# Performance work log

Hardware: AMD Instinct MI355X
Metric: run time of the kernel (lower is better)

Reference implementation:

```python
import jax, jax.numpy as jnp
import numpy as np

N_HEADS = 4
D_K = 32
C = 128
SCALE = D_K ** (-0.5)


def setup_inputs() -> dict:
    key = jax.random.key(0)
    k1, k2, k3, k4, k5 = jax.random.split(key, 5)
    x = jax.random.normal(k1, (16, C, 32, 32), dtype=jnp.float32)
    # nn.Linear(C, n_heads*d_k*3): weight [out, in], bias [out]
    Wp = jax.random.normal(k2, (N_HEADS * D_K * 3, C), dtype=jnp.float32) * (C ** -0.5)
    bp = jax.random.normal(k3, (N_HEADS * D_K * 3,), dtype=jnp.float32) * 0.01
    # nn.Linear(n_heads*d_k, C)
    Wo = jax.random.normal(k4, (C, N_HEADS * D_K), dtype=jnp.float32) * ((N_HEADS * D_K) ** -0.5)
    bo = jax.random.normal(k5, (C,), dtype=jnp.float32) * 0.01
    return {"x": x, "Wp": Wp, "bp": bp, "Wo": Wo, "bo": bo}


def reference(x, Wp, bp, Wo, bo):
    b, c, h, w = x.shape
    n = h * w
    # (b,c,h,w) -> (b, n, c); NOTE: GroupNorm from __init__ is never applied in forward.
    xf = x.reshape(b, c, n).transpose(0, 2, 1)
    qkv = (xf @ Wp.T + bp).reshape(b, n, N_HEADS, 3 * D_K)
    q, k, v = jnp.split(qkv, 3, axis=-1)  # each (b, n, heads, d_k)
    attn = jnp.einsum('bihd,bjhd->bijh', q, k) * SCALE  # (b, n, n, heads)
    # Faithful to original: softmax over LAST axis = heads axis (original code bug)
    attn = jax.nn.softmax(attn, axis=-1)
    res = jnp.einsum('bijh,bjhd->bihd', attn, v).reshape(b, n, N_HEADS * D_K)
    res = res @ Wo.T + bo + xf
    return res.transpose(0, 2, 1).reshape(b, c, h, w)
```

## Files before the change

### kernel.cpp

```cpp
#include <hip/hip_runtime.h>

typedef short s8v __attribute__((ext_vector_type(8)));
typedef float f4v __attribute__((ext_vector_type(4)));

#define NTOK 1024
#define CD 128
#define QSCALE 0.25506953149031838f

__device__ __forceinline__ ushort f2bf(float x) {
    union { float f; unsigned u; } v; v.f = x;
    unsigned u = v.u + 0x7fff + ((v.u >> 16) & 1);
    return (ushort)(u >> 16);
}
__device__ __forceinline__ float bf2f(ushort x) {
    union { unsigned u; float f; } v; v.u = ((unsigned)x) << 16;
    return v.f;
}
__device__ __forceinline__ void gl_lds16(const ushort* g, ushort* l) {
    __builtin_amdgcn_global_load_lds(
        (const __attribute__((address_space(1))) unsigned int*)(g),
        (__attribute__((address_space(3))) unsigned int*)(l), 16, 0, 0);
}
__device__ __forceinline__ unsigned cvt_pk_bf16(float lo, float hi) {
    unsigned r;
    asm("v_cvt_pk_bf16_f32 %0, %1, %2" : "=v"(r) : "v"(lo), "v"(hi));
    return r;
}

__global__ __launch_bounds__(256) void k_pre(const float* __restrict__ x,
                                             const float* __restrict__ Wp,
                                             const float* __restrict__ Wo,
                                             ushort* __restrict__ xt,
                                             ushort* __restrict__ wpre) {
    const int t = threadIdx.x;
    const int bx = blockIdx.x;
    if (bx < 256) {
        __shared__ ushort tile[128 * 68];
        const int b = bx >> 4;
        const int n0 = (bx & 15) << 6;
        #pragma unroll
        for (int p = 0; p < 8; ++p) {
            const int c = p * 16 + (t >> 4);
            const int n4 = t & 15;
            const float4 v = *(const float4*)&x[(b * CD + c) * NTOK + n0 + n4 * 4];
            ushort4 o;
            o.x = f2bf(v.x); o.y = f2bf(v.y); o.z = f2bf(v.z); o.w = f2bf(v.w);
            *(ushort4*)&tile[c * 68 + n4 * 4] = o;
        }
        __syncthreads();
        #pragma unroll
        for (int p = 0; p < 4; ++p) {
            const int nl = t >> 2;
            const int g = (t & 3) + p * 4;
            s8v tmp;
            #pragma unroll
            for (int e = 0; e < 8; ++e) tmp[e] = (short)tile[(g * 8 + e) * 68 + nl];
            const int n = n0 + nl;
            *(s8v*)&xt[(b * NTOK + n) * CD + ((g ^ (nl & 7)) * 8)] = tmp;
        }
    } else {
        const int kind = bx - 256;
        ushort* dst = wpre + kind * (CD * CD);
        for (int e = t * 4; e < CD * CD; e += 1024) {
            const int f = e >> 7, c = e & 127;
            const float* src;
            if (kind == 3) src = &Wo[f * CD + c];
            else           src = &Wp[((f >> 5) * 96 + kind * 32 + (f & 31)) * CD + c];
            const float4 v = *(const float4*)src;
            ushort4 o;
            o.x = f2bf(v.x); o.y = f2bf(v.y); o.z = f2bf(v.z); o.w = f2bf(v.w);
            *(ushort4*)&dst[f * CD + (((c >> 3) ^ (f & 7)) * 8) + (c & 7)] = o;
        }
    }
}

__global__ __launch_bounds__(256) void k_proj(const ushort* __restrict__ xt,
                                              const ushort* __restrict__ wpre,
                                              const float* __restrict__ bp,
                                              ushort* __restrict__ qb,
                                              ushort* __restrict__ kb,
                                              ushort* __restrict__ vtb) {
    __shared__ ushort Abuf[128 * 128];
    __shared__ ushort Bbuf[64 * 128];
    const int t = threadIdx.x;
    const int lane = t & 63;
    const int w = t >> 6;
    const int li = lane & 15;
    const int lg = lane >> 4;
    const int bx = blockIdx.x;
    const int kind = bx >> 8;
    const int idx = bx & 255;

    const ushort* Asrc;
    const ushort* Bsrc;
    if (kind < 2) {
        Asrc = xt + (idx >> 1) * 128 * CD;
        Bsrc = wpre + kind * (CD * CD) + (idx & 1) * 64 * CD;
    } else {
        Asrc = wpre + 2 * (CD * CD);
        Bsrc = xt + idx * 64 * CD;
    }
    {
        const ushort* ga = Asrc + w * 4096;
        ushort* la = Abuf + w * 4096;
        #pragma unroll
        for (int i = 0; i < 8; ++i) gl_lds16(ga + i * 512 + lane * 8, la + i * 512);
        const ushort* gb = Bsrc + w * 2048;
        ushort* lb = Bbuf + w * 2048;
        #pragma unroll
        for (int i = 0; i < 4; ++i) gl_lds16(gb + i * 512 + lane * 8, lb + i * 512);
    }
    __syncthreads();

    const f4v fz = {0.f, 0.f, 0.f, 0.f};
    f4v acc[2][4];
    #pragma unroll
    for (int mf = 0; mf < 2; ++mf)
        #pragma unroll
        for (int nf = 0; nf < 4; ++nf) acc[mf][nf] = fz;
    const int m_base = w * 32;
    #pragma unroll
    for (int kk = 0; kk < 4; ++kk) {
        s8v a[2], bb[4];
        #pragma unroll
        for (int mf = 0; mf < 2; ++mf) {
            const int row = m_base + mf * 16 + li;
            a[mf] = *(const s8v*)&Abuf[row * CD + (((kk * 4 + lg) ^ (row & 7)) * 8)];
        }
        #pragma unroll
        for (int nf = 0; nf < 4; ++nf) {
            const int row = nf * 16 + li;
            bb[nf] = *(const s8v*)&Bbuf[row * CD + (((kk * 4 + lg) ^ (row & 7)) * 8)];
        }
        #pragma unroll
        for (int mf = 0; mf < 2; ++mf)
            #pragma unroll
            for (int nf = 0; nf < 4; ++nf)
                acc[mf][nf] = __builtin_amdgcn_mfma_f32_16x16x32_bf16(a[mf], bb[nf], acc[mf][nf], 0, 0, 0);
    }

    if (kind < 2) {
        ushort* dst = (kind == 0) ? qb : kb;
        const int m0 = (idx >> 1) * 128;
        const int f0 = (idx & 1) * 64;
        #pragma unroll
        for (int mf = 0; mf < 2; ++mf)
            #pragma unroll
            for (int nf = 0; nf < 4; ++nf) {
                const int f = f0 + nf * 16 + li;
                const int o = (f >> 5) * 96 + kind * 32 + (f & 31);
                const float bias = bp[o];
                #pragma unroll
                for (int r = 0; r < 4; ++r) {
                    const int row = m0 + m_base + mf * 16 + lg * 4 + r;
                    float v = acc[mf][nf][r] + bias;
                    if (kind == 0) v *= QSCALE;
                    dst[row * CD + f] = f2bf(v);
                }
            }
    } else {
        const int n0g = idx * 64;
        const int b = n0g >> 10;
        const int nl0 = n0g & 1023;
        #pragma unroll
        for (int mf = 0; mf < 2; ++mf)
            #pragma unroll
            for (int r = 0; r < 4; ++r) {
                const int f = m_base + mf * 16 + lg * 4 + r;
                const int o = (f >> 5) * 96 + 64 + (f & 31);
                const float bias = bp[o];
                #pragma unroll
                for (int nf = 0; nf < 4; ++nf) {
                    const int n = nl0 + nf * 16 + li;
                    const int jl = n & 31;
                    const int np = (n & ~31) | (((jl & 15) >> 2) * 8 + (jl & 3) + ((jl >> 4) << 2));
                    vtb[(b * CD + f) * NTOK + np] = f2bf(acc[mf][nf][r] + bias);
                }
            }
    }
}

__global__ __launch_bounds__(256) void k_attn(const ushort* __restrict__ qb,
                                              const ushort* __restrict__ kb,
                                              const ushort* __restrict__ vtb,
                                              ushort* __restrict__ res4) {
    __shared__ ushort kbuf[2][32 * 128];
    __shared__ ushort vbuf[2][128 * 40];
    const int t = threadIdx.x;
    const int lane = t & 63;
    const int w = t >> 6;
    const int b = blockIdx.x;
    const int it = blockIdx.y;
    const int js = blockIdx.z;
    const int i0 = it * 64 + w * 16;
    const int li = lane & 15;
    const int lg = lane >> 4;

    s8v qf[4];
    #pragma unroll
    for (int h = 0; h < 4; ++h)
        qf[h] = *(const s8v*)&qb[(b*NTOK + i0 + li)*CD + h*32 + lg*8];

    const f4v fz = {0.f, 0.f, 0.f, 0.f};
    f4v acc[4][2];
    #pragma unroll
    for (int h = 0; h < 4; ++h) { acc[h][0] = fz; acc[h][1] = fz; }

    const int j0 = js * 256;
    const int kr0 = (w*2)*4 + (lane>>4);
    const int kr1 = (w*2+1)*4 + (lane>>4);
    const ushort* ksrc0 = &kb[(b*NTOK + j0 + kr0)*CD + (((lane&15) ^ (kr0&7))*8)];
    const ushort* ksrc1 = &kb[(b*NTOK + j0 + kr1)*CD + (((lane&15) ^ (kr1&7))*8)];
    const ushort* vptr0 = &vtb[(b*CD + (t>>2))*NTOK + j0 + (t&3)*8];
    const ushort* vptr1 = vptr0 + 64*NTOK;
    const int vwo = (t>>2)*40 + (t&3)*8;

    gl_lds16(ksrc0, &kbuf[0][w*1024]);
    gl_lds16(ksrc1, &kbuf[0][w*1024 + 512]);
    s8v v0 = *(const s8v*)vptr0;
    s8v v1 = *(const s8v*)vptr1;
    *(s8v*)&vbuf[0][vwo]          = v0;
    *(s8v*)&vbuf[0][vwo + 64*40]  = v1;
    gl_lds16(ksrc0 + 32*CD, &kbuf[1][w*1024]);
    gl_lds16(ksrc1 + 32*CD, &kbuf[1][w*1024 + 512]);
    v0 = *(const s8v*)(vptr0 + 32);
    v1 = *(const s8v*)(vptr1 + 32);
    __syncthreads();

    unsigned wv[4][4];
    {
        f4v sv[4][2];
        __builtin_amdgcn_s_setprio(1);
        #pragma unroll
        for (int h = 0; h < 4; ++h)
            #pragma unroll
            for (int jh = 0; jh < 2; ++jh) {
                const int row = jh*16 + li;
                s8v kf = *(const s8v*)&kbuf[0][row*128 + (((h*4 + lg) ^ (li & 7))*8)];
                sv[h][jh] = __builtin_amdgcn_mfma_f32_16x16x32_bf16(kf, qf[h], fz, 0, 0, 0);
            }
        __builtin_amdgcn_s_setprio(0);
        #pragma unroll
        for (int jh = 0; jh < 2; ++jh)
            #pragma unroll
            for (int r = 0; r < 4; ++r) {
                float e0 = __builtin_amdgcn_exp2f(sv[0][jh][r]);
                float e1 = __builtin_amdgcn_exp2f(sv[1][jh][r]);
                float e2 = __builtin_amdgcn_exp2f(sv[2][jh][r]);
                float e3 = __builtin_amdgcn_exp2f(sv[3][jh][r]);
                float inv = __builtin_amdgcn_rcpf(e0 + e1 + e2 + e3);
                sv[0][jh][r] = e0 * inv;
                sv[1][jh][r] = e1 * inv;
                sv[2][jh][r] = e2 * inv;
                sv[3][jh][r] = e3 * inv;
            }
        #pragma unroll
        for (int h = 0; h < 4; ++h) {
            wv[h][0] = cvt_pk_bf16(sv[h][0][0], sv[h][0][1]);
            wv[h][1] = cvt_pk_bf16(sv[h][0][2], sv[h][0][3]);
            wv[h][2] = cvt_pk_bf16(sv[h][1][0], sv[h][1][1]);
            wv[h][3] = cvt_pk_bf16(sv[h][1][2], sv[h][1][3]);
        }
    }

    #pragma unroll
    for (int tt = 1; tt <= 8; ++tt) {
        __syncthreads();
        if (tt <= 7) {
            ushort* vn = vbuf[tt & 1];
            *(s8v*)&vn[vwo]          = v0;
            *(s8v*)&vn[vwo + 64*40]  = v1;
        }
        if (tt <= 6) {
            gl_lds16(ksrc0 + (tt+1)*32*CD, &kbuf[(tt+1) & 1][w*1024]);
            gl_lds16(ksrc1 + (tt+1)*32*CD, &kbuf[(tt+1) & 1][w*1024 + 512]);
        }
        if (tt <= 6) {
            v0 = *(const s8v*)(vptr0 + (tt+1)*32);
            v1 = *(const s8v*)(vptr1 + (tt+1)*32);
        }
        f4v sv[4][2];
        if (tt <= 7) {
            const ushort* kc = kbuf[tt & 1];
            __builtin_amdgcn_s_setprio(1);
            #pragma unroll
            for (int h = 0; h < 4; ++h)
                #pragma unroll
                for (int jh = 0; jh < 2; ++jh) {
                    const int row = jh*16 + li;
                    s8v kf = *(const s8v*)&kc[row*128 + (((h*4 + lg) ^ (li & 7))*8)];
                    sv[h][jh] = __builtin_amdgcn_mfma_f32_16x16x32_bf16(kf, qf[h], fz, 0, 0, 0);
                }
            __builtin_amdgcn_s_setprio(0);
        }
        {
            const ushort* vc = vbuf[(tt - 1) & 1];
            #pragma unroll
            for (int h = 0; h < 4; ++h) {
                union { unsigned d[4]; s8v s; } av;
                av.d[0] = wv[h][0]; av.d[1] = wv[h][1];
                av.d[2] = wv[h][2]; av.d[3] = wv[h][3];
                s8v vf0 = *(const s8v*)&vc[(h*32 + li)*40 + lg*8];
                s8v vf1 = *(const s8v*)&vc[(h*32 + 16 + li)*40 + lg*8];
                __builtin_amdgcn_s_setprio(1);
                acc[h][0] = __builtin_amdgcn_mfma_f32_16x16x32_bf16(av.s, vf0, acc[h][0], 0, 0, 0);
                acc[h][1] = __builtin_amdgcn_mfma_f32_16x16x32_bf16(av.s, vf1, acc[h][1], 0, 0, 0);
                __builtin_amdgcn_s_setprio(0);
            }
        }
        if (tt <= 7) {
            #pragma unroll
            for (int jh = 0; jh < 2; ++jh)
                #pragma unroll
                for (int r = 0; r < 4; ++r) {
                    float e0 = __builtin_amdgcn_exp2f(sv[0][jh][r]);
                    float e1 = __builtin_amdgcn_exp2f(sv[1][jh][r]);
                    float e2 = __builtin_amdgcn_exp2f(sv[2][jh][r]);
                    float e3 = __builtin_amdgcn_exp2f(sv[3][jh][r]);
                    float inv = __builtin_amdgcn_rcpf(e0 + e1 + e2 + e3);
                    sv[0][jh][r] = e0 * inv;
                    sv[1][jh][r] = e1 * inv;
                    sv[2][jh][r] = e2 * inv;
                    sv[3][jh][r] = e3 * inv;
                }
            #pragma unroll
            for (int h = 0; h < 4; ++h) {
                wv[h][0] = cvt_pk_bf16(sv[h][0][0], sv[h][0][1]);
                wv[h][1] = cvt_pk_bf16(sv[h][0][2], sv[h][0][3]);
                wv[h][2] = cvt_pk_bf16(sv[h][1][0], sv[h][1][1]);
                wv[h][3] = cvt_pk_bf16(sv[h][1][2], sv[h][1][3]);
            }
        }
    }

    #pragma unroll
    for (int h = 0; h < 4; ++h)
        #pragma unroll
        for (int dh = 0; dh < 2; ++dh)
            #pragma unroll
            for (int r = 0; r < 4; ++r) {
                const int i = i0 + lg*4 + r;
                const int f = h*32 + dh*16 + li;
                res4[js*(16*NTOK*CD) + (b*NTOK + i)*CD + f] = f2bf(acc[h][dh][r]);
            }
}

__global__ __launch_bounds__(256) void k_out(const ushort* __restrict__ wpre,
                                             const ushort* __restrict__ res4,
                                             const float* __restrict__ bo,
                                             const float* __restrict__ x,
                                             float* __restrict__ out) {
    __shared__ ushort Abuf[128 * 128];
    __shared__ ushort Bbuf[64 * 128];
    const int t = threadIdx.x;
    const int lane = t & 63;
    const int w = t >> 6;
    const int li = lane & 15;
    const int lg = lane >> 4;
    const int idx = blockIdx.x;
    const int n0g = idx * 64;
    const int b = n0g >> 10;
    {
        const ushort* ga = wpre + 3 * (CD * CD) + w * 4096;
        ushort* la = Abuf + w * 4096;
        #pragma unroll
        for (int i = 0; i < 8; ++i) gl_lds16(ga + i * 512 + lane * 8, la + i * 512);
    }
    for (int u = t; u < 64 * 16; u += 256) {
        const int rl = u >> 4, g = u & 15;
        const ushort* p = &res4[(n0g + rl) * CD + g * 8];
        s8v p0 = *(const s8v*)(p);
        s8v p1 = *(const s8v*)(p + 16*NTOK*CD);
        s8v p2 = *(const s8v*)(p + 32*NTOK*CD);
        s8v p3 = *(const s8v*)(p + 48*NTOK*CD);
        s8v sm;
        #pragma unroll
        for (int e = 0; e < 8; ++e)
            sm[e] = (short)f2bf(bf2f((ushort)p0[e]) + bf2f((ushort)p1[e])
                              + bf2f((ushort)p2[e]) + bf2f((ushort)p3[e]));
        *(s8v*)&Bbuf[rl * CD + ((g ^ (rl & 7)) * 8)] = sm;
    }
    __syncthreads();

    const f4v fz = {0.f, 0.f, 0.f, 0.f};
    f4v acc[2][4];
    #pragma unroll
    for (int mf = 0; mf < 2; ++mf)
        #pragma unroll
        for (int nf = 0; nf < 4; ++nf) acc[mf][nf] = fz;
    const int m_base = w * 32;
    #pragma unroll
    for (int kk = 0; kk < 4; ++kk) {
        s8v a[2], bb[4];
        #pragma unroll
        for (int mf = 0; mf < 2; ++mf) {
            const int row = m_base + mf * 16 + li;
            a[mf] = *(const s8v*)&Abuf[row * CD + (((kk * 4 + lg) ^ (row & 7)) * 8)];
        }
        #pragma unroll
        for (int nf = 0; nf < 4; ++nf) {
            const int row = nf * 16 + li;
            bb[nf] = *(const s8v*)&Bbuf[row * CD + (((kk * 4 + lg) ^ (row & 7)) * 8)];
        }
        #pragma unroll
        for (int mf = 0; mf < 2; ++mf)
            #pragma unroll
            for (int nf = 0; nf < 4; ++nf)
                acc[mf][nf] = __builtin_amdgcn_mfma_f32_16x16x32_bf16(a[mf], bb[nf], acc[mf][nf], 0, 0, 0);
    }
    const int nl0 = n0g & 1023;
    #pragma unroll
    for (int mf = 0; mf < 2; ++mf)
        #pragma unroll
        for (int r = 0; r < 4; ++r) {
            const int o = m_base + mf * 16 + lg * 4 + r;
            const float bias = bo[o];
            #pragma unroll
            for (int nf = 0; nf < 4; ++nf) {
                const int n = nl0 + nf * 16 + li;
                const int gi = (b * CD + o) * NTOK + n;
                out[gi] = acc[mf][nf][r] + bias + x[gi];
            }
        }
}

extern "C" void kernel_launch(void* const* d_in, const int* in_sizes, int n_in,
                              void* d_out, int out_size, void* d_ws, size_t ws_size,
                              hipStream_t stream) {
    const float* x  = (const float*)d_in[0];
    const float* Wp = (const float*)d_in[1];
    const float* bp = (const float*)d_in[2];
    const float* Wo = (const float*)d_in[3];
    const float* bo = (const float*)d_in[4];
    float* out = (float*)d_out;
    ushort* xt   = (ushort*)d_ws;
    ushort* wpre = xt + 16*1024*128;
    ushort* qbw  = wpre + 4*128*128;
    ushort* kbw  = qbw + 16*1024*128;
    ushort* vtb  = kbw + 16*1024*128;
    ushort* res4 = vtb + 16*1024*128;
    k_pre <<<260, 256, 0, stream>>>(x, Wp, Wo, xt, wpre);
    k_proj<<<768, 256, 0, stream>>>(xt, wpre, bp, qbw, kbw, vtb);
    k_attn<<<dim3(16, 16, 4), 256, 0, stream>>>(qbw, kbw, vtb, res4);
    k_out <<<256, 256, 0, stream>>>(wpre, res4, bo, x, out);
}
```

Baseline: 48.87 us.

## Double-buffer partial results in k_out and accumulate split-K partials via MFMA

The output projection kernel used to sum the four split partial result buffers in registers, rounding through bf16, before one GEMM pass. It now streams each partial into a double-buffered LDS tile and runs the GEMM four times, accumulating in fp32 MFMA registers while the next partial is prefetched. This removes the scalar bf16 add and convert loop and overlaps global loads with MFMA work. In exchange it does four times the MFMA work, adds extra barriers and LDS, and changes rounding slightly because partials are no longer summed in bf16 first.

```diff
diff --git a/kernel.cpp b/kernel.cpp
--- a/kernel.cpp
+++ b/kernel.cpp
@@ -351,7 +351,7 @@
                                              const float* __restrict__ x,
                                              float* __restrict__ out) {
     __shared__ ushort Abuf[128 * 128];
-    __shared__ ushort Bbuf[64 * 128];
+    __shared__ ushort Bbuf[2][64 * 128];
     const int t = threadIdx.x;
     const int lane = t & 63;
     const int w = t >> 6;
@@ -366,20 +366,24 @@
         #pragma unroll
         for (int i = 0; i < 8; ++i) gl_lds16(ga + i * 512 + lane * 8, la + i * 512);
     }
-    for (int u = t; u < 64 * 16; u += 256) {
-        const int rl = u >> 4, g = u & 15;
-        const ushort* p = &res4[(n0g + rl) * CD + g * 8];
-        s8v p0 = *(const s8v*)(p);
-        s8v p1 = *(const s8v*)(p + 16*NTOK*CD);
-        s8v p2 = *(const s8v*)(p + 32*NTOK*CD);
-        s8v p3 = *(const s8v*)(p + 48*NTOK*CD);
-        s8v sm;
-        #pragma unroll
-        for (int e = 0; e < 8; ++e)
-            sm[e] = (short)f2bf(bf2f((ushort)p0[e]) + bf2f((ushort)p1[e])
-                              + bf2f((ushort)p2[e]) + bf2f((ushort)p3[e]));
-        *(s8v*)&Bbuf[rl * CD + ((g ^ (rl & 7)) * 8)] = sm;
-    }
+    const int rl0 = t >> 4;
+    const int g = t & 15;
+    const ushort* psrc = &res4[(n0g + rl0) * CD + g * 8];
+    const int bwo = rl0 * CD + ((g ^ (rl0 & 7)) * 8);
+
+    s8v r0, r1, r2, r3;
+    r0 = *(const s8v*)(psrc);
+    r1 = *(const s8v*)(psrc + 16*CD);
+    r2 = *(const s8v*)(psrc + 32*CD);
+    r3 = *(const s8v*)(psrc + 48*CD);
+    *(s8v*)&Bbuf[0][bwo]          = r0;
+    *(s8v*)&Bbuf[0][bwo + 16*CD]  = r1;
+    *(s8v*)&Bbuf[0][bwo + 32*CD]  = r2;
+    *(s8v*)&Bbuf[0][bwo + 48*CD]  = r3;
+    r0 = *(const s8v*)(psrc + 16*NTOK*CD);
+    r1 = *(const s8v*)(psrc + 16*NTOK*CD + 16*CD);
+    r2 = *(const s8v*)(psrc + 16*NTOK*CD + 32*CD);
+    r3 = *(const s8v*)(psrc + 16*NTOK*CD + 48*CD);
     __syncthreads();
 
     const f4v fz = {0.f, 0.f, 0.f, 0.f};
@@ -389,25 +393,46 @@
         #pragma unroll
         for (int nf = 0; nf < 4; ++nf) acc[mf][nf] = fz;
     const int m_base = w * 32;
-    #pragma unroll
-    for (int kk = 0; kk < 4; ++kk) {
-        s8v a[2], bb[4];
-        #pragma unroll
-        for (int mf = 0; mf < 2; ++mf) {
-            const int row = m_base + mf * 16 + li;
-            a[mf] = *(const s8v*)&Abuf[row * CD + (((kk * 4 + lg) ^ (row & 7)) * 8)];
-        }
-        #pragma unroll
-        for (int nf = 0; nf < 4; ++nf) {
-            const int row = nf * 16 + li;
-            bb[nf] = *(const s8v*)&Bbuf[row * CD + (((kk * 4 + lg) ^ (row & 7)) * 8)];
-        }
-        #pragma unroll
-        for (int mf = 0; mf < 2; ++mf)
-            #pragma unroll
-            for (int nf = 0; nf < 4; ++nf)
-                acc[mf][nf] = __builtin_amdgcn_mfma_f32_16x16x32_bf16(a[mf], bb[nf], acc[mf][nf], 0, 0, 0);
-    }
+
+    #pragma unroll
+    for (int p = 0; p < 4; ++p) {
+        if (p < 3) {
+            ushort* bn = Bbuf[(p + 1) & 1];
+            *(s8v*)&bn[bwo]          = r0;
+            *(s8v*)&bn[bwo + 16*CD]  = r1;
+            *(s8v*)&bn[bwo + 32*CD]  = r2;
+            *(s8v*)&bn[bwo + 48*CD]  = r3;
+        }
+        if (p < 2) {
+            const ushort* ps = psrc + (p + 2) * 16*NTOK*CD;
+            r0 = *(const s8v*)(ps);
+            r1 = *(const s8v*)(ps + 16*CD);
+            r2 = *(const s8v*)(ps + 32*CD);
+            r3 = *(const s8v*)(ps + 48*CD);
+        }
+        const ushort* bc = Bbuf[p & 1];
+        #pragma unroll
+        for (int kk = 0; kk < 4; ++kk) {
+            s8v a[2], bb[4];
+            #pragma unroll
+            for (int mf = 0; mf < 2; ++mf) {
+                const int row = m_base + mf * 16 + li;
+                a[mf] = *(const s8v*)&Abuf[row * CD + (((kk * 4 + lg) ^ (row & 7)) * 8)];
+            }
+            #pragma unroll
+            for (int nf = 0; nf < 4; ++nf) {
+                const int row = nf * 16 + li;
+                bb[nf] = *(const s8v*)&bc[row * CD + (((kk * 4 + lg) ^ (row & 7)) * 8)];
+            }
+            #pragma unroll
+            for (int mf = 0; mf < 2; ++mf)
+                #pragma unroll
+                for (int nf = 0; nf < 4; ++nf)
+                    acc[mf][nf] = __builtin_amdgcn_mfma_f32_16x16x32_bf16(a[mf], bb[nf], acc[mf][nf], 0, 0, 0);
+        }
+        __syncthreads();
+    }
+
     const int nl0 = n0g & 1023;
     #pragma unroll
     for (int mf = 0; mf < 2; ++mf)
```

Measured after the change: 49.12 us. About the same (+0.5%).
